# Kernel tuning notes

Measured on AMD Instinct MI355X. Metric: run time of the kernel, lower is better.

The kernel has to match this reference:

```python
import jax, jax.numpy as jnp
import numpy as np

EPS = 1e-5
N_HEADS = 8
NEG = -1e32


def _pos_emb(S, D):
    # CosinePositionalEmbedding: sin/cos fully overwrite the random init for even D
    pos = jnp.arange(S, dtype=jnp.float32)[:, None]
    div = jnp.exp(jnp.arange(0, D, 2, dtype=jnp.float32) * (-np.log(10000.0) / D))
    pe = jnp.zeros((S, D), dtype=jnp.float32)
    pe = pe.at[:, 0::2].set(jnp.sin(pos * div))
    pe = pe.at[:, 1::2].set(jnp.cos(pos * div))
    return pe


def _ln(x, g, b):
    mu = jnp.mean(x, axis=-1, keepdims=True)
    var = jnp.mean((x - mu) ** 2, axis=-1, keepdims=True)
    return (x - mu) / jnp.sqrt(var + EPS) * g + b


def setup_inputs() -> dict:
    key = jax.random.key(0)
    B, S, D, FF, L = 32, 512, 512, 2048, 4
    ks = jax.random.split(key, 8)
    w = 0.02
    return {
        "q_embed_data": jax.random.normal(ks[0], (B, S, D), jnp.float32),
        "qa_embed_data": jax.random.normal(ks[1], (B, S, D), jnp.float32),
        "boost_focus": jax.random.uniform(ks[2], (1,), jnp.float32),
        "Wk": w * jax.random.normal(ks[3], (L, D, D), jnp.float32),
        "bk": jnp.zeros((L, D), jnp.float32),
        "Wv": w * jax.random.normal(ks[4], (L, D, D), jnp.float32),
        "bv": jnp.zeros((L, D), jnp.float32),
        "Wo": w * jax.random.normal(ks[5], (L, D, D), jnp.float32),
        "bo": jnp.zeros((L, D), jnp.float32),
        "ln1_g": jnp.ones((L, D), jnp.float32),
        "ln1_b": jnp.zeros((L, D), jnp.float32),
        "W1": w * jax.random.normal(ks[6], (L, D, FF), jnp.float32),
        "b1": jnp.zeros((L, FF), jnp.float32),
        "W2": w * jax.random.normal(ks[7], (L, FF, D), jnp.float32),
        "b2": jnp.zeros((L, D), jnp.float32),
        "ln2_g": jnp.ones((L, D), jnp.float32),
        "ln2_b": jnp.zeros((L, D), jnp.float32),
    }


def reference(q_embed_data, qa_embed_data, boost_focus, Wk, bk, Wv, bv, Wo, bo,
              ln1_g, ln1_b, W1, b1, W2, b2, ln2_g, ln2_b):
    B, S, D = q_embed_data.shape
    L = Wk.shape[0]
    H = N_HEADS
    dk = D // H
    bf = boost_focus[0]
    pe = _pos_emb(S, D)
    x = q_embed_data + pe[None]          # query/key stream
    y = qa_embed_data + pe[None]         # value stream (fixed across blocks)
    # mask=0: triu(k=0)==0 -> only strictly past positions (j < i) allowed
    allowed = jnp.tril(jnp.ones((S, S), bool), k=-1)
    scale = 1.0 / np.sqrt(dk)
    for l in range(L):
        # kq_same=True: q and k both use k_linear on x -> identical projections
        qk = (x @ Wk[l] + bk[l]).reshape(B, S, H, dk).transpose(0, 2, 1, 3)
        v = (y @ Wv[l] + bv[l]).reshape(B, S, H, dk).transpose(0, 2, 1, 3)
        scores = jnp.einsum('bhid,bhjd->bhij', qk, qk) * scale * (1.0 + bf)
        scores = jnp.where(allowed, scores, NEG)
        probs = jax.nn.softmax(scores, axis=-1)
        probs = probs.at[:, :, 0, :].set(0.0)  # zero_pad: first query row zeroed
        attn = jnp.einsum('bhij,bhjd->bhid', probs, v)
        attn = attn.transpose(0, 2, 1, 3).reshape(B, S, D) @ Wo[l] + bo[l]
        x = _ln(x + attn, ln1_g[l], ln1_b[l])
        ff = jax.nn.relu(x @ W1[l] + b1[l]) @ W2[l] + b2[l]
        x = _ln(x + ff, ln2_g[l], ln2_b[l])
    return x
```

## Files before the change

kernel.cpp:

```cpp
#include <hip/hip_runtime.h>
#include <hip/hip_bf16.h>

typedef __bf16 bf16_t;
typedef __bf16 bf16x4 __attribute__((ext_vector_type(4)));
typedef __bf16 bf16x8 __attribute__((ext_vector_type(8)));
typedef float f32x4 __attribute__((ext_vector_type(4)));

union FragU { bf16x8 v; bf16x4 h[2]; };
union F4U { float4 v; float f[4]; };

constexpr int BB = 32, SS = 512, DD = 512, FFD = 2048, LL = 4, HH = 8;

__device__ __forceinline__ int permk(int k) {
  int g = (k >> 2) & 7;
  int pos = (g < 4) ? (g << 1) : (((g - 4) << 1) | 1);
  return (k & ~31) | (pos << 2) | (k & 3);
}

__device__ __forceinline__ void gload_lds16(const bf16_t* g, bf16_t* l) {
  __builtin_amdgcn_global_load_lds(
      (const __attribute__((address_space(1))) void*)g,
      (__attribute__((address_space(3))) void*)l, 16, 0, 0);
}

template<int N> __device__ __forceinline__ void vmwait() {
  asm volatile("s_waitcnt vmcnt(%0)" :: "n"(N) : "memory");
}
__device__ __forceinline__ void barrier_raw() {
  asm volatile("s_barrier" ::: "memory");
}

__global__ void pe_kernel(float* __restrict__ pe) {
  int idx = blockIdx.x * blockDim.x + threadIdx.x;
  if (idx >= SS * DD / 2) return;
  int p = idx % (DD / 2);
  int s = idx / (DD / 2);
  float div = expf((float)(2 * p) * (-9.210340371976184f / (float)DD));
  float a = (float)s * div;
  pe[s * DD + 2 * p]     = sinf(a);
  pe[s * DD + 2 * p + 1] = cosf(a);
}

__global__ __launch_bounds__(256) void tcast_kernel(const float* __restrict__ src,
                                                    bf16_t* __restrict__ dst,
                                                    int K, int N) {
  __shared__ float tile[32][33];
  size_t mat = (size_t)blockIdx.z * (size_t)K * (size_t)N;
  int k0 = blockIdx.y * 32, n0 = blockIdx.x * 32;
  int t = threadIdx.x;
  int r = t >> 3, c4 = (t & 7) * 4;
  const float4 v = *reinterpret_cast<const float4*>(&src[mat + (size_t)(k0 + r) * N + n0 + c4]);
  tile[r][c4 + 0] = v.x; tile[r][c4 + 1] = v.y; tile[r][c4 + 2] = v.z; tile[r][c4 + 3] = v.w;
  __syncthreads();
  bf16x4 o;
  o[0] = (bf16_t)tile[c4 + 0][r];
  o[1] = (bf16_t)tile[c4 + 1][r];
  o[2] = (bf16_t)tile[c4 + 2][r];
  o[3] = (bf16_t)tile[c4 + 3][r];
  *reinterpret_cast<bf16x4*>(&dst[mat + permk((n0 + r) * K + k0 + c4)]) = o;
}

__global__ void addpe_kernel(const float* __restrict__ q, const float* __restrict__ qa,
                             const float* __restrict__ pe,
                             float* __restrict__ x, bf16_t* __restrict__ xb,
                             bf16_t* __restrict__ yb) {
  int i = blockIdx.x * blockDim.x + threadIdx.x;
  int pei = i & (SS * DD / 4 - 1);
  float4 pv = reinterpret_cast<const float4*>(pe)[pei];
  float4 qv = reinterpret_cast<const float4*>(q)[i];
  float4 av = reinterpret_cast<const float4*>(qa)[i];
  float4 xv = make_float4(qv.x + pv.x, qv.y + pv.y, qv.z + pv.z, qv.w + pv.w);
  float4 yv = make_float4(av.x + pv.x, av.y + pv.y, av.z + pv.z, av.w + pv.w);
  reinterpret_cast<float4*>(x)[i] = xv;
  bf16x4 xo, yo;
  xo[0] = (bf16_t)xv.x; xo[1] = (bf16_t)xv.y; xo[2] = (bf16_t)xv.z; xo[3] = (bf16_t)xv.w;
  yo[0] = (bf16_t)yv.x; yo[1] = (bf16_t)yv.y; yo[2] = (bf16_t)yv.z; yo[3] = (bf16_t)yv.w;
  int kp = permk(4 * i);
  *reinterpret_cast<bf16x4*>(&xb[kp]) = xo;
  *reinterpret_cast<bf16x4*>(&yb[kp]) = yo;
}

template<int OMODE, bool RELU>
__global__ __launch_bounds__(256, 2) void gemm_kernel(const bf16_t* __restrict__ A,
                                                      const bf16_t* __restrict__ Bt,
                                                      const float* __restrict__ bias,
                                                      void* __restrict__ Cout,
                                                      int N, int K, int nnt) {
  __shared__ bf16_t a_s[2][128 * 64];
  __shared__ bf16_t b_s[2][128 * 64];
  const int t = threadIdx.x;
  const int nwg = gridDim.x;
  const int bid = blockIdx.x;
  const int wg = (bid & 7) * (nwg >> 3) + (bid >> 3);
  const int m0 = (wg / nnt) * 128, n0 = (wg % nnt) * 128;
  const int l = t & 63, w = t >> 6, g = l >> 4, ln = l & 15;
  const int wm = (w >> 1) * 64, wn = (w & 1) * 64;
  const int tr = t >> 3;
  const int bsrc = ((t & 7) ^ (tr & 7)) * 8;
  const bf16_t* Asrc = A + (size_t)(m0 + tr) * K + bsrc;
  const bf16_t* Bsrc = Bt + (size_t)(n0 + tr) * K + bsrc;
  const size_t rstr = (size_t)32 * K;
  const int x0 = (g ^ (ln & 7)) * 8;
  const int x1 = ((4 + g) ^ (ln & 7)) * 8;

  auto STAGE = [&](int p, int T) {
    const int k0 = T << 6;
#pragma unroll
    for (int i = 0; i < 4; i++) gload_lds16(Asrc + k0 + i * rstr, &a_s[p][(i * 256 + t) * 8]);
#pragma unroll
    for (int i = 0; i < 4; i++) gload_lds16(Bsrc + k0 + i * rstr, &b_s[p][(i * 256 + t) * 8]);
  };

  f32x4 acc[4][4] = {};
  const int NT = K >> 6;
  STAGE(0, 0);
  STAGE(1, 1);
  for (int T = 0; T < NT; T++) {
    const int p = T & 1;
    if (T + 1 < NT) vmwait<8>(); else vmwait<0>();
    barrier_raw();
    __builtin_amdgcn_sched_barrier(0);
#pragma unroll
    for (int kc = 0; kc < 2; kc++) {
      const int xo = kc ? x1 : x0;
      FragU fa[4], fb[4];
#pragma unroll
      for (int mi = 0; mi < 4; mi++)
        fa[mi].v = *reinterpret_cast<const bf16x8*>(&a_s[p][(wm + mi * 16 + ln) * 64 + xo]);
#pragma unroll
      for (int ni = 0; ni < 4; ni++)
        fb[ni].v = *reinterpret_cast<const bf16x8*>(&b_s[p][(wn + ni * 16 + ln) * 64 + xo]);
      __builtin_amdgcn_s_setprio(1);
#pragma unroll
      for (int mi = 0; mi < 4; mi++)
#pragma unroll
        for (int ni = 0; ni < 4; ni++)
          acc[mi][ni] = __builtin_amdgcn_mfma_f32_16x16x32_bf16(fa[mi].v, fb[ni].v, acc[mi][ni], 0, 0, 0);
      __builtin_amdgcn_s_setprio(0);
    }
    __builtin_amdgcn_sched_barrier(0);
    barrier_raw();
    if (T + 2 < NT) STAGE(p, T + 2);
  }

  if constexpr (OMODE == 2) {
    const int brow = m0 >> 9;
    const int s0b = (m0 & 511) + wm;
    bf16_t* vout = reinterpret_cast<bf16_t*>(Cout);
#pragma unroll
    for (int ni = 0; ni < 4; ni++) {
      const int d = n0 + wn + ni * 16 + ln;
      const float bv = bias[d];
      const int h = d >> 6, dd = d & 63;
      bf16_t* vrow = vout + ((size_t)((brow * HH + h) * 64 + dd)) * SS;
#pragma unroll
      for (int mi = 0; mi < 4; mi++) {
        const int s0 = s0b + mi * 16 + g * 4;
        const int jt = s0 >> 6, jj = s0 & 63;
        const int js = jj >> 5, half = (jj >> 4) & 1;
        const int blkx = (js * 4 + g) ^ (dd & 7);
        bf16x4 o;
#pragma unroll
        for (int r = 0; r < 4; r++) o[r] = (bf16_t)(acc[mi][ni][r] + bv);
        *reinterpret_cast<bf16x4*>(&vrow[jt * 64 + blkx * 8 + half * 4]) = o;
      }
    }
  } else {
#pragma unroll
    for (int ni = 0; ni < 4; ni++) {
      const int col = n0 + wn + ni * 16 + ln;
      const float bv = bias[col];
      const int colp = (OMODE == 1) ? permk(col) : col;
#pragma unroll
      for (int mi = 0; mi < 4; mi++)
#pragma unroll
        for (int r = 0; r < 4; r++) {
          int row = m0 + wm + mi * 16 + g * 4 + r;
          float o = acc[mi][ni][r] + bv;
          if (RELU) o = fmaxf(o, 0.f);
          if (OMODE == 1)
            reinterpret_cast<bf16_t*>(Cout)[(size_t)row * N + colp] = (bf16_t)o;
          else
            reinterpret_cast<float*>(Cout)[(size_t)row * N + col] = o;
        }
    }
  }
}

__global__ __launch_bounds__(256) void ln_kernel(const float* __restrict__ xin,
                                                 const float* __restrict__ addv,
                                                 const float* __restrict__ gamma,
                                                 const float* __restrict__ beta,
                                                 float* __restrict__ xout,
                                                 bf16_t* __restrict__ xbout) {
  int row = blockIdx.x * 4 + (threadIdx.x >> 6);
  int l = threadIdx.x & 63;
  const float* px = xin + (size_t)row * DD;
  const float* pa = addv + (size_t)row * DD;
  float vals[8];
  float s = 0.f;
#pragma unroll
  for (int i = 0; i < 2; i++) {
    float4 a = reinterpret_cast<const float4*>(px)[l * 2 + i];
    float4 b = reinterpret_cast<const float4*>(pa)[l * 2 + i];
    vals[i * 4 + 0] = a.x + b.x;
    vals[i * 4 + 1] = a.y + b.y;
    vals[i * 4 + 2] = a.z + b.z;
    vals[i * 4 + 3] = a.w + b.w;
  }
#pragma unroll
  for (int j = 0; j < 8; j++) s += vals[j];
#pragma unroll
  for (int off = 1; off < 64; off <<= 1) s += __shfl_xor(s, off, 64);
  float mean = s * (1.f / DD);
  float sq = 0.f;
#pragma unroll
  for (int j = 0; j < 8; j++) { float d = vals[j] - mean; sq += d * d; }
#pragma unroll
  for (int off = 1; off < 64; off <<= 1) sq += __shfl_xor(sq, off, 64);
  float rstd = rsqrtf(sq * (1.f / DD) + 1e-5f);
#pragma unroll
  for (int i = 0; i < 2; i++) {
    F4U o; bf16x4 ob;
#pragma unroll
    for (int j = 0; j < 4; j++) {
      int colj = l * 8 + i * 4 + j;
      float v = (vals[i * 4 + j] - mean) * rstd * gamma[colj] + beta[colj];
      o.f[j] = v;
      ob[j] = (bf16_t)v;
    }
    reinterpret_cast<float4*>(xout + (size_t)row * DD)[l * 2 + i] = o.v;
    *reinterpret_cast<bf16x4*>(&xbout[(size_t)row * DD + permk(l * 8 + i * 4)]) = ob;
  }
}

__global__ __launch_bounds__(256) void attn_kernel(const bf16_t* __restrict__ qk,
                                                   const bf16_t* __restrict__ vtg,
                                                   bf16_t* __restrict__ outp,
                                                   const float* __restrict__ bfp) {
  __shared__ bf16_t k_s[64 * 64];
  __shared__ bf16_t v_t[64 * 64];
  const int bx = blockIdx.x, h = blockIdx.y, b = blockIdx.z;
  const int t = threadIdx.x, l = t & 63, w = t >> 6, g = l >> 4, ln = l & 15;
  const float sc = 0.125f * (1.f + bfp[0]);
  const size_t base = ((size_t)b * SS) * DD + h * 64;
  const bf16_t* vbase = vtg + ((size_t)((b * HH + h) * 64)) * SS;
  const int NQT = SS / 64;

  for (int pass = 0; pass < 2; pass++) {
    const int qt = pass ? (NQT - 1 - bx) : bx;
    const int i0 = qt * 64;
    FragU qB[2];
    {
      const bf16_t* qp = qk + base + (size_t)(i0 + w * 16 + ln) * DD;
      qB[0].v = *reinterpret_cast<const bf16x8*>(&qp[g * 8]);
      qB[1].v = *reinterpret_cast<const bf16x8*>(&qp[32 + g * 8]);
    }
    float m = -1e30f, lrow = 0.f;
    f32x4 acc[4] = {};
    const int iql = w * 16 + ln;

    for (int kt = 0; kt <= qt; kt++) {
      const int j0 = kt * 64;
      __syncthreads();
      {
        int c1 = t + 256;
        int jr0 = t >> 3, bb0 = t & 7;
        int jr1 = c1 >> 3, bb1 = c1 & 7;
        gload_lds16(qk + base + (size_t)(j0 + jr0) * DD + ((bb0 ^ (jr0 & 7)) * 8), &k_s[t * 8]);
        gload_lds16(qk + base + (size_t)(j0 + jr1) * DD + ((bb1 ^ (jr1 & 7)) * 8), &k_s[c1 * 8]);
        gload_lds16(vbase + (size_t)jr0 * SS + j0 + bb0 * 8, &v_t[t * 8]);
        gload_lds16(vbase + (size_t)jr1 * SS + j0 + bb1 * 8, &v_t[c1 * 8]);
      }
      asm volatile("s_waitcnt vmcnt(0)" ::: "memory");
      __syncthreads();
      f32x4 sfr[4] = {};
#pragma unroll
      for (int ks = 0; ks < 2; ks++)
#pragma unroll
        for (int nj = 0; nj < 4; nj++) {
          int jc = nj * 16 + ln;
          FragU ka;
          ka.v = *reinterpret_cast<const bf16x8*>(&k_s[jc * 64 + (((ks * 4 + g) ^ (jc & 7)) * 8)]);
          sfr[nj] = __builtin_amdgcn_mfma_f32_16x16x32_bf16(ka.v, qB[ks].v, sfr[nj], 0, 0, 0);
        }
      if (kt == qt) {
#pragma unroll
        for (int nj = 0; nj < 4; nj++)
#pragma unroll
          for (int r = 0; r < 4; r++)
            if (nj * 16 + g * 4 + r >= iql) sfr[nj][r] = -1e30f;
      }
      float pm = -1e30f;
#pragma unroll
      for (int nj = 0; nj < 4; nj++)
#pragma unroll
        for (int r = 0; r < 4; r++) pm = fmaxf(pm, sfr[nj][r]);
      pm = fmaxf(pm, __shfl_xor(pm, 16, 64));
      pm = fmaxf(pm, __shfl_xor(pm, 32, 64));
      float mnew = fmaxf(m, pm);
      float fac = __expf(sc * (m - mnew));
      m = mnew;
      float ps = 0.f;
#pragma unroll
      for (int nj = 0; nj < 4; nj++)
#pragma unroll
        for (int r = 0; r < 4; r++) {
          float p = __expf(sc * (sfr[nj][r] - m));
          sfr[nj][r] = p;
          ps += p;
        }
      ps += __shfl_xor(ps, 16, 64);
      ps += __shfl_xor(ps, 32, 64);
      lrow = lrow * fac + ps;
      float facr[4];
#pragma unroll
      for (int r = 0; r < 4; r++) facr[r] = __shfl(fac, g * 4 + r, 64);
#pragma unroll
      for (int nd = 0; nd < 4; nd++)
#pragma unroll
        for (int r = 0; r < 4; r++) acc[nd][r] *= facr[r];
      FragU pa[2];
#pragma unroll
      for (int js = 0; js < 2; js++)
#pragma unroll
        for (int kk = 0; kk < 4; kk++) {
          pa[js].v[kk]     = (bf16_t)sfr[js * 2][kk];
          pa[js].v[kk + 4] = (bf16_t)sfr[js * 2 + 1][kk];
        }
#pragma unroll
      for (int js = 0; js < 2; js++)
#pragma unroll
        for (int nd = 0; nd < 4; nd++) {
          int d = nd * 16 + ln;
          FragU vb;
          vb.v = *reinterpret_cast<const bf16x8*>(&v_t[d * 64 + (((js * 4 + g) ^ (d & 7)) * 8)]);
          acc[nd] = __builtin_amdgcn_mfma_f32_16x16x32_bf16(pa[js].v, vb.v, acc[nd], 0, 0, 0);
        }
    }
    float lr[4];
#pragma unroll
    for (int r = 0; r < 4; r++) lr[r] = __shfl(lrow, g * 4 + r, 64);
    const int orow0 = i0 + w * 16 + g * 4;
#pragma unroll
    for (int nd = 0; nd < 4; nd++) {
      const int colp = permk(nd * 16 + ln);
#pragma unroll
      for (int r = 0; r < 4; r++) {
        int grow = orow0 + r;
        float o = (grow > 0 && lr[r] > 0.f) ? acc[nd][r] / lr[r] : 0.f;
        outp[base + (size_t)grow * DD + colp] = (bf16_t)o;
      }
    }
  }
}

extern "C" void kernel_launch(void* const* d_in, const int* in_sizes, int n_in,
                              void* d_out, int out_size, void* d_ws, size_t ws_size,
                              hipStream_t stream) {
  const float* q_emb  = (const float*)d_in[0];
  const float* qa_emb = (const float*)d_in[1];
  const float* bfp    = (const float*)d_in[2];
  const float* Wk  = (const float*)d_in[3];
  const float* bk  = (const float*)d_in[4];
  const float* Wv  = (const float*)d_in[5];
  const float* bv  = (const float*)d_in[6];
  const float* Wo  = (const float*)d_in[7];
  const float* bo  = (const float*)d_in[8];
  const float* g1  = (const float*)d_in[9];
  const float* be1 = (const float*)d_in[10];
  const float* W1  = (const float*)d_in[11];
  const float* b1  = (const float*)d_in[12];
  const float* W2  = (const float*)d_in[13];
  const float* b2  = (const float*)d_in[14];
  const float* g2  = (const float*)d_in[15];
  const float* be2 = (const float*)d_in[16];
  float* out = (float*)d_out;
  (void)in_sizes; (void)n_in; (void)out_size; (void)ws_size;

  char* wsp = (char*)d_ws;
  size_t off = 0;
  auto alloc = [&](size_t bytes) -> void* {
    void* p = wsp + off;
    off += (bytes + 255) & ~(size_t)255;
    return p;
  };
  const size_t BSD = (size_t)BB * SS * DD;
  float*  pe   = (float*) alloc((size_t)SS * DD * 4);
  float*  x    = (float*) alloc(BSD * 4);
  float*  tmp  = (float*) alloc(BSD * 4);
  bf16_t* xb   = (bf16_t*)alloc(BSD * 2);
  bf16_t* yb   = (bf16_t*)alloc(BSD * 2);
  bf16_t* qkb  = (bf16_t*)alloc(BSD * 2);
  bf16_t* vtg  = (bf16_t*)alloc(BSD * 2);
  bf16_t* atb  = (bf16_t*)alloc(BSD * 2);
  bf16_t* h1   = (bf16_t*)alloc((size_t)BB * SS * FFD * 2);
  bf16_t* Wkb  = (bf16_t*)alloc((size_t)LL * DD * DD * 2);
  bf16_t* Wvb  = (bf16_t*)alloc((size_t)LL * DD * DD * 2);
  bf16_t* Wob  = (bf16_t*)alloc((size_t)LL * DD * DD * 2);
  bf16_t* W1b  = (bf16_t*)alloc((size_t)LL * DD * FFD * 2);
  bf16_t* W2b  = (bf16_t*)alloc((size_t)LL * FFD * DD * 2);

  pe_kernel<<<(SS * DD / 2 + 255) / 256, 256, 0, stream>>>(pe);
  tcast_kernel<<<dim3(DD / 32, DD / 32, LL), 256, 0, stream>>>(Wk, Wkb, DD, DD);
  tcast_kernel<<<dim3(DD / 32, DD / 32, LL), 256, 0, stream>>>(Wv, Wvb, DD, DD);
  tcast_kernel<<<dim3(DD / 32, DD / 32, LL), 256, 0, stream>>>(Wo, Wob, DD, DD);
  tcast_kernel<<<dim3(FFD / 32, DD / 32, LL), 256, 0, stream>>>(W1, W1b, DD, FFD);
  tcast_kernel<<<dim3(DD / 32, FFD / 32, LL), 256, 0, stream>>>(W2, W2b, FFD, DD);
  addpe_kernel<<<(int)(BSD / 4 / 256), 256, 0, stream>>>(q_emb, qa_emb, pe, x, xb, yb);

  const int M = BB * SS;
  const int nD = (M / 128) * (DD / 128);
  const int nF = (M / 128) * (FFD / 128);
  dim3 gA(SS / 128, HH, BB);
  for (int layer = 0; layer < LL; layer++) {
    const bf16_t* Wkl = Wkb + (size_t)layer * DD * DD;
    const bf16_t* Wvl = Wvb + (size_t)layer * DD * DD;
    const bf16_t* Wol = Wob + (size_t)layer * DD * DD;
    const bf16_t* W1l = W1b + (size_t)layer * DD * FFD;
    const bf16_t* W2l = W2b + (size_t)layer * FFD * DD;
    gemm_kernel<1, false><<<nD, 256, 0, stream>>>(xb, Wkl, bk + layer * DD, qkb, DD, DD, DD / 128);
    gemm_kernel<2, false><<<nD, 256, 0, stream>>>(yb, Wvl, bv + layer * DD, vtg, DD, DD, DD / 128);
    attn_kernel<<<gA, 256, 0, stream>>>(qkb, vtg, atb, bfp);
    gemm_kernel<0, false><<<nD, 256, 0, stream>>>(atb, Wol, bo + layer * DD, tmp, DD, DD, DD / 128);
    ln_kernel<<<M / 4, 256, 0, stream>>>(x, tmp, g1 + layer * DD, be1 + layer * DD, x, xb);
    gemm_kernel<1, true><<<nF, 256, 0, stream>>>(xb, W1l, b1 + layer * FFD, h1, FFD, DD, FFD / 128);
    gemm_kernel<0, false><<<nD, 256, 0, stream>>>(h1, W2l, b2 + layer * DD, tmp, DD, FFD, DD / 128);
    float* xo = (layer == LL - 1) ? out : x;
    ln_kernel<<<M / 4, 256, 0, stream>>>(x, tmp, g2 + layer * DD, be2 + layer * DD, xo, xb);
  }
}
```

Before: 828.5 us.

## Keep residual stream in bf16 permuted layout and double-buffer attention K/V

Drops the fp32 residual copy and fp32 GEMM outputs. Wo and W2 now write bf16 in the permuted layout, and a new LayerNorm reads and writes that permuted bf16 directly, using pre-permuted gamma/beta and unpermuting only for the final fp32 output. This cuts HBM traffic in the LN and GEMM epilogues. The attention kernel also double-buffers K/V tiles in LDS so the next tile's loads overlap compute. The cost is reduced precision: the residual is rounded to bf16 every layer.

```diff
diff --git a/kernel.cpp b/kernel.cpp
--- a/kernel.cpp
+++ b/kernel.cpp
@@ -29,6 +29,8 @@
 __device__ __forceinline__ void barrier_raw() {
   asm volatile("s_barrier" ::: "memory");
 }
+
+#define MFMA_ACC(d, a, b) d = __builtin_amdgcn_mfma_f32_16x16x32_bf16((a).v, (b).v, d, 0, 0, 0)
 
 __global__ void pe_kernel(float* __restrict__ pe) {
   int idx = blockIdx.x * blockDim.x + threadIdx.x;
@@ -39,6 +41,16 @@
   float a = (float)s * div;
   pe[s * DD + 2 * p]     = sinf(a);
   pe[s * DD + 2 * p + 1] = cosf(a);
+}
+
+__global__ void gbperm_kernel(const float* __restrict__ g1, const float* __restrict__ b1,
+                              const float* __restrict__ g2, const float* __restrict__ b2,
+                              float* __restrict__ g1p, float* __restrict__ b1p,
+                              float* __restrict__ g2p, float* __restrict__ b2p) {
+  int idx = blockIdx.x * 256 + threadIdx.x;
+  if (idx >= LL * DD) return;
+  int p = (idx & ~511) | permk(idx & 511);
+  g1p[p] = g1[idx]; b1p[p] = b1[idx]; g2p[p] = g2[idx]; b2p[p] = b2[idx];
 }
 
 __global__ __launch_bounds__(256) void tcast_kernel(const float* __restrict__ src,
@@ -62,19 +74,17 @@
 
 __global__ void addpe_kernel(const float* __restrict__ q, const float* __restrict__ qa,
                              const float* __restrict__ pe,
-                             float* __restrict__ x, bf16_t* __restrict__ xb,
-                             bf16_t* __restrict__ yb) {
+                             bf16_t* __restrict__ xb, bf16_t* __restrict__ yb) {
   int i = blockIdx.x * blockDim.x + threadIdx.x;
   int pei = i & (SS * DD / 4 - 1);
   float4 pv = reinterpret_cast<const float4*>(pe)[pei];
   float4 qv = reinterpret_cast<const float4*>(q)[i];
   float4 av = reinterpret_cast<const float4*>(qa)[i];
-  float4 xv = make_float4(qv.x + pv.x, qv.y + pv.y, qv.z + pv.z, qv.w + pv.w);
-  float4 yv = make_float4(av.x + pv.x, av.y + pv.y, av.z + pv.z, av.w + pv.w);
-  reinterpret_cast<float4*>(x)[i] = xv;
   bf16x4 xo, yo;
-  xo[0] = (bf16_t)xv.x; xo[1] = (bf16_t)xv.y; xo[2] = (bf16_t)xv.z; xo[3] = (bf16_t)xv.w;
-  yo[0] = (bf16_t)yv.x; yo[1] = (bf16_t)yv.y; yo[2] = (bf16_t)yv.z; yo[3] = (bf16_t)yv.w;
+  xo[0] = (bf16_t)(qv.x + pv.x); xo[1] = (bf16_t)(qv.y + pv.y);
+  xo[2] = (bf16_t)(qv.z + pv.z); xo[3] = (bf16_t)(qv.w + pv.w);
+  yo[0] = (bf16_t)(av.x + pv.x); yo[1] = (bf16_t)(av.y + pv.y);
+  yo[2] = (bf16_t)(av.z + pv.z); yo[3] = (bf16_t)(av.w + pv.w);
   int kp = permk(4 * i);
   *reinterpret_cast<bf16x4*>(&xb[kp]) = xo;
   *reinterpret_cast<bf16x4*>(&yb[kp]) = yo;
@@ -135,7 +145,7 @@
       for (int mi = 0; mi < 4; mi++)
 #pragma unroll
         for (int ni = 0; ni < 4; ni++)
-          acc[mi][ni] = __builtin_amdgcn_mfma_f32_16x16x32_bf16(fa[mi].v, fb[ni].v, acc[mi][ni], 0, 0, 0);
+          MFMA_ACC(acc[mi][ni], fa[mi], fb[ni]);
       __builtin_amdgcn_s_setprio(0);
     }
     __builtin_amdgcn_sched_barrier(0);
@@ -170,7 +180,7 @@
     for (int ni = 0; ni < 4; ni++) {
       const int col = n0 + wn + ni * 16 + ln;
       const float bv = bias[col];
-      const int colp = (OMODE == 1) ? permk(col) : col;
+      const int colp = permk(col);
 #pragma unroll
       for (int mi = 0; mi < 4; mi++)
 #pragma unroll
@@ -178,38 +188,29 @@
           int row = m0 + wm + mi * 16 + g * 4 + r;
           float o = acc[mi][ni][r] + bv;
           if (RELU) o = fmaxf(o, 0.f);
-          if (OMODE == 1)
-            reinterpret_cast<bf16_t*>(Cout)[(size_t)row * N + colp] = (bf16_t)o;
-          else
-            reinterpret_cast<float*>(Cout)[(size_t)row * N + col] = o;
+          reinterpret_cast<bf16_t*>(Cout)[(size_t)row * N + colp] = (bf16_t)o;
         }
     }
   }
 }
 
-__global__ __launch_bounds__(256) void ln_kernel(const float* __restrict__ xin,
-                                                 const float* __restrict__ addv,
-                                                 const float* __restrict__ gamma,
-                                                 const float* __restrict__ beta,
-                                                 float* __restrict__ xout,
-                                                 bf16_t* __restrict__ xbout) {
+template<bool FINAL>
+__global__ __launch_bounds__(256) void lnp_kernel(const bf16_t* __restrict__ xb,
+                                                  const bf16_t* __restrict__ tb,
+                                                  const float* __restrict__ gp,
+                                                  const float* __restrict__ bp,
+                                                  bf16_t* __restrict__ xbo,
+                                                  float* __restrict__ fout) {
   int row = blockIdx.x * 4 + (threadIdx.x >> 6);
   int l = threadIdx.x & 63;
-  const float* px = xin + (size_t)row * DD;
-  const float* pa = addv + (size_t)row * DD;
+  size_t base = (size_t)row * DD + l * 8;
+  FragU xv, tv;
+  xv.v = *reinterpret_cast<const bf16x8*>(&xb[base]);
+  tv.v = *reinterpret_cast<const bf16x8*>(&tb[base]);
   float vals[8];
   float s = 0.f;
 #pragma unroll
-  for (int i = 0; i < 2; i++) {
-    float4 a = reinterpret_cast<const float4*>(px)[l * 2 + i];
-    float4 b = reinterpret_cast<const float4*>(pa)[l * 2 + i];
-    vals[i * 4 + 0] = a.x + b.x;
-    vals[i * 4 + 1] = a.y + b.y;
-    vals[i * 4 + 2] = a.z + b.z;
-    vals[i * 4 + 3] = a.w + b.w;
-  }
-#pragma unroll
-  for (int j = 0; j < 8; j++) s += vals[j];
+  for (int j = 0; j < 8; j++) { vals[j] = (float)xv.v[j] + (float)tv.v[j]; s += vals[j]; }
 #pragma unroll
   for (int off = 1; off < 64; off <<= 1) s += __shfl_xor(s, off, 64);
   float mean = s * (1.f / DD);
@@ -219,18 +220,29 @@
 #pragma unroll
   for (int off = 1; off < 64; off <<= 1) sq += __shfl_xor(sq, off, 64);
   float rstd = rsqrtf(sq * (1.f / DD) + 1e-5f);
-#pragma unroll
-  for (int i = 0; i < 2; i++) {
-    F4U o; bf16x4 ob;
-#pragma unroll
-    for (int j = 0; j < 4; j++) {
-      int colj = l * 8 + i * 4 + j;
-      float v = (vals[i * 4 + j] - mean) * rstd * gamma[colj] + beta[colj];
-      o.f[j] = v;
-      ob[j] = (bf16_t)v;
-    }
-    reinterpret_cast<float4*>(xout + (size_t)row * DD)[l * 2 + i] = o.v;
-    *reinterpret_cast<bf16x4*>(&xbout[(size_t)row * DD + permk(l * 8 + i * 4)]) = ob;
+  F4U g0, g1q, b0, b1q;
+  g0.v  = *reinterpret_cast<const float4*>(&gp[l * 8]);
+  g1q.v = *reinterpret_cast<const float4*>(&gp[l * 8 + 4]);
+  b0.v  = *reinterpret_cast<const float4*>(&bp[l * 8]);
+  b1q.v = *reinterpret_cast<const float4*>(&bp[l * 8 + 4]);
+  float ov[8];
+#pragma unroll
+  for (int j = 0; j < 4; j++) ov[j]     = (vals[j] - mean) * rstd * g0.f[j] + b0.f[j];
+#pragma unroll
+  for (int j = 0; j < 4; j++) ov[4 + j] = (vals[4 + j] - mean) * rstd * g1q.f[j] + b1q.f[j];
+  if (FINAL) {
+    int c = l >> 2, i = l & 3;
+    F4U o0, o1;
+#pragma unroll
+    for (int j = 0; j < 4; j++) { o0.f[j] = ov[j]; o1.f[j] = ov[4 + j]; }
+    float* fr = fout + (size_t)row * DD + c * 32 + 4 * i;
+    *reinterpret_cast<float4*>(fr) = o0.v;
+    *reinterpret_cast<float4*>(fr + 16) = o1.v;
+  } else {
+    FragU ob;
+#pragma unroll
+    for (int j = 0; j < 8; j++) ob.v[j] = (bf16_t)ov[j];
+    *reinterpret_cast<bf16x8*>(&xbo[base]) = ob.v;
   }
 }
 
@@ -238,8 +250,8 @@
                                                    const bf16_t* __restrict__ vtg,
                                                    bf16_t* __restrict__ outp,
                                                    const float* __restrict__ bfp) {
-  __shared__ bf16_t k_s[64 * 64];
-  __shared__ bf16_t v_t[64 * 64];
+  __shared__ bf16_t k_s[2][64 * 64];
+  __shared__ bf16_t v_t[2][64 * 64];
   const int bx = blockIdx.x, h = blockIdx.y, b = blockIdx.z;
   const int t = threadIdx.x, l = t & 63, w = t >> 6, g = l >> 4, ln = l & 15;
   const float sc = 0.125f * (1.f + bfp[0]);
@@ -247,9 +259,20 @@
   const bf16_t* vbase = vtg + ((size_t)((b * HH + h) * 64)) * SS;
   const int NQT = SS / 64;
 
+  auto STAGEKV = [&](int q, int j0) {
+    int c1 = t + 256;
+    int jr0 = t >> 3, bb0 = t & 7;
+    int jr1 = c1 >> 3, bb1 = c1 & 7;
+    gload_lds16(qk + base + (size_t)(j0 + jr0) * DD + ((bb0 ^ (jr0 & 7)) * 8), &k_s[q][t * 8]);
+    gload_lds16(qk + base + (size_t)(j0 + jr1) * DD + ((bb1 ^ (jr1 & 7)) * 8), &k_s[q][c1 * 8]);
+    gload_lds16(vbase + (size_t)jr0 * SS + j0 + bb0 * 8, &v_t[q][t * 8]);
+    gload_lds16(vbase + (size_t)jr1 * SS + j0 + bb1 * 8, &v_t[q][c1 * 8]);
+  };
+
   for (int pass = 0; pass < 2; pass++) {
     const int qt = pass ? (NQT - 1 - bx) : bx;
     const int i0 = qt * 64;
+    STAGEKV(0, 0);
     FragU qB[2];
     {
       const bf16_t* qp = qk + base + (size_t)(i0 + w * 16 + ln) * DD;
@@ -262,18 +285,11 @@
 
     for (int kt = 0; kt <= qt; kt++) {
       const int j0 = kt * 64;
-      __syncthreads();
-      {
-        int c1 = t + 256;
-        int jr0 = t >> 3, bb0 = t & 7;
-        int jr1 = c1 >> 3, bb1 = c1 & 7;
-        gload_lds16(qk + base + (size_t)(j0 + jr0) * DD + ((bb0 ^ (jr0 & 7)) * 8), &k_s[t * 8]);
-        gload_lds16(qk + base + (size_t)(j0 + jr1) * DD + ((bb1 ^ (jr1 & 7)) * 8), &k_s[c1 * 8]);
-        gload_lds16(vbase + (size_t)jr0 * SS + j0 + bb0 * 8, &v_t[t * 8]);
-        gload_lds16(vbase + (size_t)jr1 * SS + j0 + bb1 * 8, &v_t[c1 * 8]);
-      }
-      asm volatile("s_waitcnt vmcnt(0)" ::: "memory");
-      __syncthreads();
+      const int p = kt & 1;
+      if (kt < qt) { STAGEKV(p ^ 1, j0 + 64); vmwait<4>(); }
+      else vmwait<0>();
+      barrier_raw();
+      __builtin_amdgcn_sched_barrier(0);
       f32x4 sfr[4] = {};
 #pragma unroll
       for (int ks = 0; ks < 2; ks++)
@@ -281,7 +297,7 @@
         for (int nj = 0; nj < 4; nj++) {
           int jc = nj * 16 + ln;
           FragU ka;
-          ka.v = *reinterpret_cast<const bf16x8*>(&k_s[jc * 64 + (((ks * 4 + g) ^ (jc & 7)) * 8)]);
+          ka.v = *reinterpret_cast<const bf16x8*>(&k_s[p][jc * 64 + (((ks * 4 + g) ^ (jc & 7)) * 8)]);
           sfr[nj] = __builtin_amdgcn_mfma_f32_16x16x32_bf16(ka.v, qB[ks].v, sfr[nj], 0, 0, 0);
         }
       if (kt == qt) {
@@ -306,9 +322,9 @@
       for (int nj = 0; nj < 4; nj++)
 #pragma unroll
         for (int r = 0; r < 4; r++) {
-          float p = __expf(sc * (sfr[nj][r] - m));
-          sfr[nj][r] = p;
-          ps += p;
+          float p2 = __expf(sc * (sfr[nj][r] - m));
+          sfr[nj][r] = p2;
+          ps += p2;
         }
       ps += __shfl_xor(ps, 16, 64);
       ps += __shfl_xor(ps, 32, 64);
@@ -334,9 +350,10 @@
         for (int nd = 0; nd < 4; nd++) {
           int d = nd * 16 + ln;
           FragU vb;
-          vb.v = *reinterpret_cast<const bf16x8*>(&v_t[d * 64 + (((js * 4 + g) ^ (d & 7)) * 8)]);
+          vb.v = *reinterpret_cast<const bf16x8*>(&v_t[p][d * 64 + (((js * 4 + g) ^ (d & 7)) * 8)]);
           acc[nd] = __builtin_amdgcn_mfma_f32_16x16x32_bf16(pa[js].v, vb.v, acc[nd], 0, 0, 0);
         }
+      barrier_raw();
     }
     float lr[4];
 #pragma unroll
@@ -387,14 +404,17 @@
   };
   const size_t BSD = (size_t)BB * SS * DD;
   float*  pe   = (float*) alloc((size_t)SS * DD * 4);
-  float*  x    = (float*) alloc(BSD * 4);
-  float*  tmp  = (float*) alloc(BSD * 4);
   bf16_t* xb   = (bf16_t*)alloc(BSD * 2);
   bf16_t* yb   = (bf16_t*)alloc(BSD * 2);
   bf16_t* qkb  = (bf16_t*)alloc(BSD * 2);
   bf16_t* vtg  = (bf16_t*)alloc(BSD * 2);
   bf16_t* atb  = (bf16_t*)alloc(BSD * 2);
+  bf16_t* tmpb = (bf16_t*)alloc(BSD * 2);
   bf16_t* h1   = (bf16_t*)alloc((size_t)BB * SS * FFD * 2);
+  float*  g1p  = (float*) alloc((size_t)LL * DD * 4);
+  float*  b1p  = (float*) alloc((size_t)LL * DD * 4);
+  float*  g2p  = (float*) alloc((size_t)LL * DD * 4);
+  float*  b2p  = (float*) alloc((size_t)LL * DD * 4);
   bf16_t* Wkb  = (bf16_t*)alloc((size_t)LL * DD * DD * 2);
   bf16_t* Wvb  = (bf16_t*)alloc((size_t)LL * DD * DD * 2);
   bf16_t* Wob  = (bf16_t*)alloc((size_t)LL * DD * DD * 2);
@@ -402,12 +422,13 @@
   bf16_t* W2b  = (bf16_t*)alloc((size_t)LL * FFD * DD * 2);
 
   pe_kernel<<<(SS * DD / 2 + 255) / 256, 256, 0, stream>>>(pe);
+  gbperm_kernel<<<(LL * DD + 255) / 256, 256, 0, stream>>>(g1, be1, g2, be2, g1p, b1p, g2p, b2p);
   tcast_kernel<<<dim3(DD / 32, DD / 32, LL), 256, 0, stream>>>(Wk, Wkb, DD, DD);
   tcast_kernel<<<dim3(DD / 32, DD / 32, LL), 256, 0, stream>>>(Wv, Wvb, DD, DD);
   tcast_kernel<<<dim3(DD / 32, DD / 32, LL), 256, 0, stream>>>(Wo, Wob, DD, DD);
   tcast_kernel<<<dim3(FFD / 32, DD / 32, LL), 256, 0, stream>>>(W1, W1b, DD, FFD);
   tcast_kernel<<<dim3(DD / 32, FFD / 32, LL), 256, 0, stream>>>(W2, W2b, FFD, DD);
-  addpe_kernel<<<(int)(BSD / 4 / 256), 256, 0, stream>>>(q_emb, qa_emb, pe, x, xb, yb);
+  addpe_kernel<<<(int)(BSD / 4 / 256), 256, 0, stream>>>(q_emb, qa_emb, pe, xb, yb);
 
   const int M = BB * SS;
   const int nD = (M / 128) * (DD / 128);
@@ -422,11 +443,13 @@
     gemm_kernel<1, false><<<nD, 256, 0, stream>>>(xb, Wkl, bk + layer * DD, qkb, DD, DD, DD / 128);
     gemm_kernel<2, false><<<nD, 256, 0, stream>>>(yb, Wvl, bv + layer * DD, vtg, DD, DD, DD / 128);
     attn_kernel<<<gA, 256, 0, stream>>>(qkb, vtg, atb, bfp);
-    gemm_kernel<0, false><<<nD, 256, 0, stream>>>(atb, Wol, bo + layer * DD, tmp, DD, DD, DD / 128);
-    ln_kernel<<<M / 4, 256, 0, stream>>>(x, tmp, g1 + layer * DD, be1 + layer * DD, x, xb);
+    gemm_kernel<1, false><<<nD, 256, 0, stream>>>(atb, Wol, bo + layer * DD, tmpb, DD, DD, DD / 128);
+    lnp_kernel<false><<<M / 4, 256, 0, stream>>>(xb, tmpb, g1p + layer * DD, b1p + layer * DD, xb, nullptr);
     gemm_kernel<1, true><<<nF, 256, 0, stream>>>(xb, W1l, b1 + layer * FFD, h1, FFD, DD, FFD / 128);
-    gemm_kernel<0, false><<<nD, 256, 0, stream>>>(h1, W2l, b2 + layer * DD, tmp, DD, FFD, DD / 128);
-    float* xo = (layer == LL - 1) ? out : x;
-    ln_kernel<<<M / 4, 256, 0, stream>>>(x, tmp, g2 + layer * DD, be2 + layer * DD, xo, xb);
+    gemm_kernel<1, false><<<nD, 256, 0, stream>>>(h1, W2l, b2 + layer * DD, tmpb, DD, FFD, DD / 128);
+    if (layer == LL - 1)
+      lnp_kernel<true><<<M / 4, 256, 0, stream>>>(xb, tmpb, g2p + layer * DD, b2p + layer * DD, nullptr, out);
+    else
+      lnp_kernel<false><<<M / 4, 256, 0, stream>>>(xb, tmpb, g2p + layer * DD, b2p + layer * DD, xb, nullptr);
   }
 }
```

Result: faster. 761.8 us (-8.1%).
